# Performance work log

Measured on AMD Instinct MI355X. Metric: run time of the kernel, lower is better.

Reference implementation:

```python
import jax, jax.numpy as jnp
import numpy as np

N = 10000          # nodes
E_RAND = 320000    # random edges (avg degree 32)
F_IN = 512         # nfeat
HID = 256          # args.hid
HEADS = 8          # args.head
FH = HID // HEADS  # 32 per head
NCLASS = 40
TAU = 0.5
LAMDA = 0.5
K = 2


def setup_inputs() -> dict:
    key = jax.random.key(0)
    ks = jax.random.split(key, 16)
    # edge list: random edges + self-loops (so every dst segment is non-empty)
    src = jnp.concatenate([jax.random.randint(ks[0], (E_RAND,), 0, N), jnp.arange(N)])
    dst = jnp.concatenate([jax.random.randint(ks[1], (E_RAND,), 0, N), jnp.arange(N)])
    s = 0.05  # small init scale keeps exp() in attention/bind_loss stable
    return {
        "x": jax.random.normal(ks[2], (N, F_IN), jnp.float32),
        "src": src, "dst": dst,
        "W0": jax.random.normal(ks[3], (F_IN, HEADS, FH), jnp.float32) * s,
        "a0s": jax.random.normal(ks[4], (HEADS, FH), jnp.float32) * s,
        "a0d": jax.random.normal(ks[5], (HEADS, FH), jnp.float32) * s,
        "W1": jax.random.normal(ks[6], (HID, HEADS, FH), jnp.float32) * s,
        "a1s": jax.random.normal(ks[7], (HEADS, FH), jnp.float32) * s,
        "a1d": jax.random.normal(ks[8], (HEADS, FH), jnp.float32) * s,
        "W2": jax.random.normal(ks[9], (HID, HEADS, FH), jnp.float32) * s,
        "a2s": jax.random.normal(ks[10], (HEADS, FH), jnp.float32) * s,
        "a2d": jax.random.normal(ks[11], (HEADS, FH), jnp.float32) * s,
        "Wout": jax.random.normal(ks[12], (HID, HEADS, NCLASS), jnp.float32) * s,
        "aos": jax.random.normal(ks[13], (HEADS, NCLASS), jnp.float32) * s,
        "aod": jax.random.normal(ks[14], (HEADS, NCLASS), jnp.float32) * s,
    }


def _gat_layer(x, W, a_s, a_d, src, dst):
    """Sparse multi-head GAT layer: gather -> edge softmax -> scatter."""
    n = x.shape[0]
    h = jnp.einsum('nf,fhd->nhd', x, W)              # [N,H,Fh]
    es = jnp.sum(h * a_s, axis=-1)                    # [N,H]
    ed = jnp.sum(h * a_d, axis=-1)                    # [N,H]
    e = jax.nn.leaky_relu(es[src] + ed[dst], 0.2)     # [E,H]
    m = jax.ops.segment_max(e, dst, num_segments=n)   # per-dst max (stable softmax)
    w = jnp.exp(e - m[dst])
    z = jax.ops.segment_sum(w, dst, num_segments=n)
    alpha = w / z[dst]                                # [E,H]
    return jax.ops.segment_sum(alpha[:, :, None] * h[src], dst, num_segments=n)  # [N,H,Fh]


def _bind_loss(z):
    # z1 == z2 == z in the original call site: refl_sim == between_sim
    zn = z / jnp.maximum(jnp.linalg.norm(z, axis=1, keepdims=True), 1e-12)
    S = jnp.exp(jnp.matmul(zn, zn.T) / TAU)           # [N,N]
    d = jnp.diagonal(S)
    off = jnp.sum(S, axis=1) - d                      # masked (off-diagonal) row sum
    CT = -jnp.log(d / (off + off))                    # neg_c2.sum + neg_c3.sum
    return jnp.mean(CT)


def reference(x, src, dst, W0, a0s, a0d, W1, a1s, a1d, W2, a2s, a2d, Wout, aos, aod):
    layers = [(W0, a0s, a0d), (W1, a1s, a1d), (W2, a2s, a2d)]
    last = x
    loss = jnp.float32(0.0)
    for i, (W, as_, ad_) in enumerate(layers):
        cur = jax.nn.elu(_gat_layer(last, W, as_, ad_, src, dst))
        cur = cur.reshape(cur.shape[0], -1)           # concat heads -> [N, HID]
        if i > 0:
            beta = LAMDA / (i + 2)                    # MaskLayer(last, cur, lamda, i+2)
            cur = beta * last + (1.0 - beta) * cur
            if i % K == 0:
                loss = loss + _bind_loss(cur)
        last = cur
    out = _gat_layer(last, Wout, aos, aod, src, dst).mean(axis=1)  # avg heads -> [N,C]
    return (jax.nn.log_softmax(out, axis=1), loss)
```

## Files before the change

kernel.cpp:

```cpp
#include <hip/hip_runtime.h>
#include <hip/hip_bf16.h>
#include <math.h>

#define NN_F_IN   512
#define NN_HID    256
#define NN_HEADS  8
#define NN_FH     32
#define NN_NCLASS 40
#define TAU_F     0.5f
#define LAMDA_F   0.5f
#define ZN_SCALE  1.6986436f

typedef __attribute__((ext_vector_type(8))) short bf16x8;
typedef __attribute__((ext_vector_type(4))) float f32x4;

typedef __attribute__((address_space(1))) unsigned int gu32_t;
typedef __attribute__((address_space(3))) unsigned int lu32_t;

static __device__ __forceinline__ float lrelu02(float x) { return x >= 0.f ? x : 0.2f * x; }
static __device__ __forceinline__ float elu1(float x)    { return x > 0.f ? x : expm1f(x); }
static __device__ __forceinline__ float b2f(unsigned short u) {
    unsigned int x = ((unsigned int)u) << 16;
    return __uint_as_float(x);
}
static __device__ __forceinline__ unsigned short f2b(float f) {
    __hip_bfloat16 hb = __float2bfloat16(f);
    return *reinterpret_cast<unsigned short*>(&hb);
}

__global__ void prep_kernel(const float* __restrict__ x,
                            const float* __restrict__ W0, const float* __restrict__ W1,
                            const float* __restrict__ W2, const float* __restrict__ Wo,
                            unsigned short* __restrict__ Xb,
                            unsigned short* __restrict__ Wt0, unsigned short* __restrict__ Wt1,
                            unsigned short* __restrict__ Wt2, unsigned short* __restrict__ Wto,
                            int n4X) {
    int i = blockIdx.x * 256 + threadIdx.x;
    if (i < n4X) {
        float4 v = *(const float4*)(x + (size_t)i * 4);
        ushort4 o;
        o.x = f2b(v.x); o.y = f2b(v.y); o.z = f2b(v.z); o.w = f2b(v.w);
        *(ushort4*)(Xb + (size_t)i * 4) = o;
        return;
    }
    i -= n4X;
    if (i < 256 * 512) {
        int np = i >> 9, k = i & 511;
        Wt0[i] = f2b(W0[(size_t)k * 256 + np]);
        return;
    }
    i -= 256 * 512;
    if (i < 256 * 256) {
        int np = i >> 8, k = i & 255;
        Wt1[i] = f2b(W1[(size_t)k * 256 + np]);
        return;
    }
    i -= 256 * 256;
    if (i < 256 * 256) {
        int np = i >> 8, k = i & 255;
        Wt2[i] = f2b(W2[(size_t)k * 256 + np]);
        return;
    }
    i -= 256 * 256;
    if (i < 384 * 256) {
        int np = i >> 8, k = i & 255;
        Wto[i] = f2b(np < 320 ? Wo[(size_t)k * 320 + np] : 0.f);
    }
}

__global__ __launch_bounds__(256) void fc_attn_mfma(
    const unsigned short* __restrict__ A, const unsigned short* __restrict__ B,
    unsigned short* __restrict__ H, const float* __restrict__ As_,
    const float* __restrict__ Ad_, float* __restrict__ es, float* __restrict__ ed,
    int M, int K) {
    const int ldH = 256;
    int t = threadIdx.x, lane = t & 63, wid = t >> 6;
    int wrow = wid >> 1, wcol = wid & 1;
    int l15 = lane & 15, lg = lane >> 4;
    int mbase = blockIdx.y * 64 + wrow * 32;
    int nbase = blockIdx.x * 64 + wcol * 32;

    const unsigned short* Ap[2];
    const unsigned short* Bp[2];
#pragma unroll
    for (int m = 0; m < 2; ++m) {
        int rr = mbase + m * 16 + l15;
        if (rr > M - 1) rr = M - 1;
        Ap[m] = A + (size_t)rr * K + lg * 8;
        Bp[m] = B + (size_t)(nbase + m * 16 + l15) * K + lg * 8;
    }
    f32x4 acc[2][2];
#pragma unroll
    for (int m = 0; m < 2; ++m)
#pragma unroll
        for (int nn = 0; nn < 2; ++nn)
#pragma unroll
            for (int r = 0; r < 4; ++r) acc[m][nn][r] = 0.f;

    bf16x8 aP[2], bP[2], aQ[2], bQ[2];
#pragma unroll
    for (int m = 0; m < 2; ++m) {
        aP[m] = *(const bf16x8*)(Ap[m]);
        bP[m] = *(const bf16x8*)(Bp[m]);
    }
    int nhalf = K >> 6;
    int kk = 32;
    for (int it = 0; it < nhalf; ++it) {
#pragma unroll
        for (int m = 0; m < 2; ++m) {
            aQ[m] = *(const bf16x8*)(Ap[m] + kk);
            bQ[m] = *(const bf16x8*)(Bp[m] + kk);
        }
#pragma unroll
        for (int m = 0; m < 2; ++m)
#pragma unroll
            for (int nn = 0; nn < 2; ++nn)
                acc[m][nn] = __builtin_amdgcn_mfma_f32_16x16x32_bf16(aP[m], bP[nn], acc[m][nn], 0, 0, 0);
        if (it + 1 < nhalf) {
#pragma unroll
            for (int m = 0; m < 2; ++m) {
                aP[m] = *(const bf16x8*)(Ap[m] + kk + 32);
                bP[m] = *(const bf16x8*)(Bp[m] + kk + 32);
            }
        }
#pragma unroll
        for (int m = 0; m < 2; ++m)
#pragma unroll
            for (int nn = 0; nn < 2; ++nn)
                acc[m][nn] = __builtin_amdgcn_mfma_f32_16x16x32_bf16(aQ[m], bQ[nn], acc[m][nn], 0, 0, 0);
        kk += 64;
    }
#pragma unroll
    for (int m = 0; m < 2; ++m) {
#pragma unroll
        for (int nn = 0; nn < 2; ++nn) {
            int col = nbase + nn * 16 + l15;
#pragma unroll
            for (int r = 0; r < 4; ++r) {
                int row = mbase + m * 16 + lg * 4 + r;
                if (row < M) H[(size_t)row * ldH + col] = f2b(acc[m][nn][r]);
            }
        }
    }
    int hh = blockIdx.x * 2 + wcol;
    float a0 = As_[hh * 32 + l15], a1 = As_[hh * 32 + 16 + l15];
    float d0 = Ad_[hh * 32 + l15], d1 = Ad_[hh * 32 + 16 + l15];
#pragma unroll
    for (int m = 0; m < 2; ++m) {
#pragma unroll
        for (int r = 0; r < 4; ++r) {
            float ps = acc[m][0][r] * a0 + acc[m][1][r] * a1;
            float pd = acc[m][0][r] * d0 + acc[m][1][r] * d1;
            ps += __shfl_xor(ps, 1, 64); pd += __shfl_xor(pd, 1, 64);
            ps += __shfl_xor(ps, 2, 64); pd += __shfl_xor(pd, 2, 64);
            ps += __shfl_xor(ps, 4, 64); pd += __shfl_xor(pd, 4, 64);
            ps += __shfl_xor(ps, 8, 64); pd += __shfl_xor(pd, 8, 64);
            if (l15 == 0) {
                int row = mbase + m * 16 + lg * 4 + r;
                if (row < M) {
                    es[row * NN_HEADS + hh] = ps;
                    ed[row * NN_HEADS + hh] = pd;
                }
            }
        }
    }
}

__global__ __launch_bounds__(256) void fc_mfma(const unsigned short* __restrict__ A,
                                               const unsigned short* __restrict__ B,
                                               unsigned short* __restrict__ H,
                                               int M, int K, int ncols, int ldH) {
    int t = threadIdx.x, lane = t & 63, wid = t >> 6;
    int wrow = wid >> 1, wcol = wid & 1;
    int l15 = lane & 15, lg = lane >> 4;
    int mbase = blockIdx.y * 64 + wrow * 32;
    int nbase = blockIdx.x * 64 + wcol * 32;

    const unsigned short* Ap[2];
    const unsigned short* Bp[2];
#pragma unroll
    for (int m = 0; m < 2; ++m) {
        int rr = mbase + m * 16 + l15;
        if (rr > M - 1) rr = M - 1;
        Ap[m] = A + (size_t)rr * K + lg * 8;
        Bp[m] = B + (size_t)(nbase + m * 16 + l15) * K + lg * 8;
    }
    f32x4 acc[2][2];
#pragma unroll
    for (int m = 0; m < 2; ++m)
#pragma unroll
        for (int nn = 0; nn < 2; ++nn)
#pragma unroll
            for (int r = 0; r < 4; ++r) acc[m][nn][r] = 0.f;

    bf16x8 aP[2], bP[2], aQ[2], bQ[2];
#pragma unroll
    for (int m = 0; m < 2; ++m) {
        aP[m] = *(const bf16x8*)(Ap[m]);
        bP[m] = *(const bf16x8*)(Bp[m]);
    }
    int nhalf = K >> 6;
    int kk = 32;
    for (int it = 0; it < nhalf; ++it) {
#pragma unroll
        for (int m = 0; m < 2; ++m) {
            aQ[m] = *(const bf16x8*)(Ap[m] + kk);
            bQ[m] = *(const bf16x8*)(Bp[m] + kk);
        }
#pragma unroll
        for (int m = 0; m < 2; ++m)
#pragma unroll
            for (int nn = 0; nn < 2; ++nn)
                acc[m][nn] = __builtin_amdgcn_mfma_f32_16x16x32_bf16(aP[m], bP[nn], acc[m][nn], 0, 0, 0);
        if (it + 1 < nhalf) {
#pragma unroll
            for (int m = 0; m < 2; ++m) {
                aP[m] = *(const bf16x8*)(Ap[m] + kk + 32);
                bP[m] = *(const bf16x8*)(Bp[m] + kk + 32);
            }
        }
#pragma unroll
        for (int m = 0; m < 2; ++m)
#pragma unroll
            for (int nn = 0; nn < 2; ++nn)
                acc[m][nn] = __builtin_amdgcn_mfma_f32_16x16x32_bf16(aQ[m], bQ[nn], acc[m][nn], 0, 0, 0);
        kk += 64;
    }
#pragma unroll
    for (int m = 0; m < 2; ++m) {
#pragma unroll
        for (int nn = 0; nn < 2; ++nn) {
            int col = nbase + nn * 16 + l15;
            if (col >= ncols) continue;
#pragma unroll
            for (int r = 0; r < 4; ++r) {
                int row = mbase + m * 16 + lg * 4 + r;
                if (row < M) H[(size_t)row * ldH + col] = f2b(acc[m][nn][r]);
            }
        }
    }
}

__global__ void attn_kernel(const unsigned short* __restrict__ Hm, const float* __restrict__ As,
                            const float* __restrict__ Ad, float* __restrict__ es,
                            float* __restrict__ ed, int n, int df) {
    int idx = blockIdx.x * blockDim.x + threadIdx.x;
    if (idx >= n * NN_HEADS) return;
    int nn = idx / NN_HEADS, hh = idx - nn * NN_HEADS;
    const unsigned short* hp = Hm + (size_t)nn * NN_HEADS * df + hh * df;
    const float* ap = As + hh * df;
    const float* bp = Ad + hh * df;
    float s1 = 0.f, s2 = 0.f;
    for (int d = 0; d < df; d += 4) {
        ushort4 hv = *(const ushort4*)(hp + d);
        float4 av = *(const float4*)(ap + d);
        float4 bv = *(const float4*)(bp + d);
        float h0 = b2f(hv.x), h1 = b2f(hv.y), h2 = b2f(hv.z), h3 = b2f(hv.w);
        s1 += h0 * av.x + h1 * av.y + h2 * av.z + h3 * av.w;
        s2 += h0 * bv.x + h1 * bv.y + h2 * bv.z + h3 * bv.w;
    }
    es[idx] = s1;
    ed[idx] = s2;
}

__global__ __launch_bounds__(256) void edge_wz(
    const float* __restrict__ es, const float* __restrict__ ed,
    const int* __restrict__ csr_src, const int* __restrict__ row_start,
    float* __restrict__ wC, float* __restrict__ zinv, int n) {
    int lane = threadIdx.x & 63;
    int nn   = blockIdx.x * 4 + (threadIdx.x >> 6);
    if (nn >= n) return;
    int s0 = row_start[nn], s1 = row_start[nn + 1];
    int h    = lane & 7;
    int slot = lane >> 3;
    float edh = ed[nn * NN_HEADS + h];
    float z = 0.f;
    for (int e = s0 + slot; e < s1; e += 8) {
        int sv = csr_src[e];
        float w = __expf(lrelu02(es[sv * NN_HEADS + h] + edh));
        wC[(size_t)e * NN_HEADS + h] = w;
        z += w;
    }
    z += __shfl_xor(z, 8, 64);
    z += __shfl_xor(z, 16, 64);
    z += __shfl_xor(z, 32, 64);
    if (slot == 0) zinv[nn * NN_HEADS + h] = 1.f / z;
}

__global__ void count_kernel(const int* __restrict__ dst, int* __restrict__ counts, int E) {
    int e = blockIdx.x * blockDim.x + threadIdx.x;
    if (e < E) atomicAdd(&counts[dst[e]], 1);
}

__global__ void scan_kernel(const int* __restrict__ counts, int* __restrict__ row_start,
                            int* __restrict__ cursor, int n) {
    __shared__ int s[1024];
    int t  = threadIdx.x;
    int ch = (n + 1023) / 1024;
    int lo = t * ch;
    int sum = 0;
    for (int j = 0; j < ch; ++j) {
        int i = lo + j;
        if (i < n) sum += counts[i];
    }
    s[t] = sum;
    __syncthreads();
    for (int off = 1; off < 1024; off <<= 1) {
        int v = 0;
        if (t >= off) v = s[t - off];
        __syncthreads();
        s[t] += v;
        __syncthreads();
    }
    int run = (t == 0) ? 0 : s[t - 1];
    for (int j = 0; j < ch; ++j) {
        int i = lo + j;
        if (i < n) {
            row_start[i] = run;
            cursor[i] = run;
            run += counts[i];
        }
    }
    if (t == 1023) row_start[n] = s[1023];
}

__global__ void scatter_kernel(const int* __restrict__ src, const int* __restrict__ dst,
                               int* __restrict__ cursor, int* __restrict__ csr_src, int E) {
    int e = blockIdx.x * blockDim.x + threadIdx.x;
    if (e < E) {
        int d   = dst[e];
        int pos = atomicAdd(&cursor[d], 1);
        csr_src[pos] = src[e];
    }
}

__global__ __launch_bounds__(256) void gather_hidden(
    const unsigned short* __restrict__ Hm, const float* __restrict__ es,
    const float* __restrict__ ed, const int* __restrict__ csr_src,
    const int* __restrict__ row_start, const unsigned short* __restrict__ last,
    unsigned short* __restrict__ out, int n, float beta,
    unsigned short* __restrict__ znb, float* __restrict__ dvec) {
    int lane = threadIdx.x & 63;
    int nn   = blockIdx.x * 4 + (threadIdx.x >> 6);
    if (nn >= n) return;
    int s0 = row_start[nn], s1 = row_start[nn + 1];
    int h2 = lane >> 3;
    float edh = ed[nn * NN_HEADS + h2];

    float zacc = 0.f;
    float a0 = 0.f, a1 = 0.f, a2 = 0.f, a3 = 0.f;
    int fullEnd = s0 + ((s1 - s0) & ~7);
    int e = s0;
    for (; e < fullEnd; e += 8) {
        int idx[8];
        float q[8];
#pragma unroll
        for (int j = 0; j < 8; ++j) idx[j] = csr_src[e + j];
#pragma unroll
        for (int j = 0; j < 8; ++j) q[j] = es[idx[j] * NN_HEADS + h2];
        ushort4 r[8];
#pragma unroll
        for (int j = 0; j < 8; ++j) r[j] = *(const ushort4*)&Hm[(size_t)idx[j] * NN_HID + lane * 4];
#pragma unroll
        for (int j = 0; j < 8; ++j) {
            float w = __expf(lrelu02(q[j] + edh));
            zacc += w;
            a0 += w * b2f(r[j].x); a1 += w * b2f(r[j].y);
            a2 += w * b2f(r[j].z); a3 += w * b2f(r[j].w);
        }
    }
    if (e < s1) {
        int c = s1 - e;
        int idx[8];
        float q[8];
#pragma unroll
        for (int j = 0; j < 8; ++j) idx[j] = csr_src[(j < c) ? e + j : e];
#pragma unroll
        for (int j = 0; j < 8; ++j) q[j] = es[idx[j] * NN_HEADS + h2];
        ushort4 r[8];
#pragma unroll
        for (int j = 0; j < 8; ++j) r[j] = *(const ushort4*)&Hm[(size_t)idx[j] * NN_HID + lane * 4];
#pragma unroll
        for (int j = 0; j < 8; ++j) {
            if (j < c) {
                float w = __expf(lrelu02(q[j] + edh));
                zacc += w;
                a0 += w * b2f(r[j].x); a1 += w * b2f(r[j].y);
                a2 += w * b2f(r[j].z); a3 += w * b2f(r[j].w);
            }
        }
    }
    float zi = 1.f / zacc;
    float v0 = elu1(a0 * zi), v1 = elu1(a1 * zi), v2 = elu1(a2 * zi), v3 = elu1(a3 * zi);
    if (beta >= 0.f) {
        ushort4 lv = *(const ushort4*)&last[(size_t)nn * NN_HID + lane * 4];
        v0 = beta * b2f(lv.x) + (1.f - beta) * v0;
        v1 = beta * b2f(lv.y) + (1.f - beta) * v1;
        v2 = beta * b2f(lv.z) + (1.f - beta) * v2;
        v3 = beta * b2f(lv.w) + (1.f - beta) * v3;
    }
    ushort4 o;
    o.x = f2b(v0); o.y = f2b(v1); o.z = f2b(v2); o.w = f2b(v3);
    *(ushort4*)&out[(size_t)nn * NN_HID + lane * 4] = o;

    if (znb) {
        float ss = v0 * v0 + v1 * v1 + v2 * v2 + v3 * v3;
        ss += __shfl_xor(ss, 1, 64);
        ss += __shfl_xor(ss, 2, 64);
        ss += __shfl_xor(ss, 4, 64);
        ss += __shfl_xor(ss, 8, 64);
        ss += __shfl_xor(ss, 16, 64);
        ss += __shfl_xor(ss, 32, 64);
        float m = fmaxf(sqrtf(ss), 1e-12f);
        float sc = ZN_SCALE / m;
        ushort4 zo;
        zo.x = f2b(v0 * sc); zo.y = f2b(v1 * sc);
        zo.z = f2b(v2 * sc); zo.w = f2b(v3 * sc);
        *(ushort4*)&znb[(size_t)nn * NN_HID + lane * 4] = zo;
        if (lane == 0) dvec[nn] = __expf((ss / (m * m)) * (1.f / TAU_F));
    }
}

__global__ void gather_final(const unsigned short* __restrict__ Hm, const float* __restrict__ wC,
                             const float* __restrict__ zinv, const int* __restrict__ csr_src,
                             const int* __restrict__ row_start, float* __restrict__ dout, int n) {
    int nn = blockIdx.x;
    __shared__ float accs[NN_HEADS * NN_NCLASS];
    int t = threadIdx.x;
    int s0 = row_start[nn], s1 = row_start[nn + 1];
    int hh = t / NN_NCLASS;
    float acc = 0.f;
    const int LD = NN_HEADS * NN_NCLASS;
    int fullEnd = s0 + ((s1 - s0) & ~7);
    int e = s0;
    for (; e < fullEnd; e += 8) {
        int idx[8];
        float wv[8];
#pragma unroll
        for (int j = 0; j < 8; ++j) {
            idx[j] = csr_src[e + j];
            wv[j]  = wC[(size_t)(e + j) * NN_HEADS + hh];
        }
        float v[8];
#pragma unroll
        for (int j = 0; j < 8; ++j) v[j] = b2f(Hm[(size_t)idx[j] * LD + t]);
#pragma unroll
        for (int j = 0; j < 8; ++j) acc += wv[j] * v[j];
    }
    if (e < s1) {
        int c = s1 - e;
        int idx[8];
        float wv[8];
#pragma unroll
        for (int j = 0; j < 8; ++j) {
            int p = (j < c) ? e + j : e;
            idx[j] = csr_src[p];
            wv[j]  = wC[(size_t)p * NN_HEADS + hh];
        }
        float v[8];
#pragma unroll
        for (int j = 0; j < 8; ++j) v[j] = b2f(Hm[(size_t)idx[j] * LD + t]);
#pragma unroll
        for (int j = 0; j < 8; ++j) {
            if (j < c) acc += wv[j] * v[j];
        }
    }
    accs[t] = acc * zinv[nn * NN_HEADS + hh];
    __syncthreads();
    if (t < 64) {
        float v = -INFINITY;
        if (t < NN_NCLASS) {
            float sacc = 0.f;
#pragma unroll
            for (int h2 = 0; h2 < NN_HEADS; ++h2) sacc += accs[h2 * NN_NCLASS + t];
            v = sacc * (1.f / NN_HEADS);
        }
        float mx = v;
#pragma unroll
        for (int o = 1; o < 64; o <<= 1) mx = fmaxf(mx, __shfl_xor(mx, o, 64));
        float ex = (t < NN_NCLASS) ? expf(v - mx) : 0.f;
        float se = ex;
#pragma unroll
        for (int o = 1; o < 64; o <<= 1) se += __shfl_xor(se, o, 64);
        if (t < NN_NCLASS) dout[(size_t)nn * NN_NCLASS + t] = (v - mx) - logf(se);
    }
}

__global__ __launch_bounds__(256) void gram_mfma(const short* __restrict__ znb,
                                                 float* __restrict__ P2d, int n,
                                                 int T, int nwg, int Npad) {
    __shared__ short As[2][128 * 32];
    __shared__ short Bs[2][128 * 32];

    int b = blockIdx.x;
    int q = nwg >> 3, r8 = nwg & 7, xc = b & 7, oo = b >> 3;
    int sid = (xc < r8 ? xc * (q + 1) : r8 * (q + 1) + (xc - r8) * q) + oo;
    int bi = 0, rem = sid;
    while (rem >= T - bi) { rem -= T - bi; ++bi; }
    int bj = bi + rem;
    int i0 = bi * 128, j0 = bj * 128;

    int t    = threadIdx.x;
    int lane = t & 63;
    int wid  = t >> 6;
    int wrow = wid >> 1, wcol = wid & 1;
    int l15  = lane & 15, lg = lane >> 4;

    int srow0 = 16 * (2 * wid + 0) + (lane >> 2);
    int srow1 = 16 * (2 * wid + 1) + (lane >> 2);
    int kc    = lane & 3;
    int kc0   = kc ^ ((srow0 >> 1) & 3);
    int kc1   = kc ^ ((srow1 >> 1) & 3);
    const short* gA0 = znb + (size_t)(i0 + srow0) * NN_HID + kc0 * 8;
    const short* gA1 = znb + (size_t)(i0 + srow1) * NN_HID + kc1 * 8;
    const short* gB0 = znb + (size_t)(j0 + srow0) * NN_HID + kc0 * 8;
    const short* gB1 = znb + (size_t)(j0 + srow1) * NN_HID + kc1 * 8;
    int ldst0 = (2 * wid + 0) * 512 + lane * 8;
    int ldst1 = (2 * wid + 1) * 512 + lane * 8;

    auto stage = [&](int buf, int s) {
        int ko = s * 32;
        __builtin_amdgcn_global_load_lds((gu32_t*)(gA0 + ko), (lu32_t*)(&As[buf][ldst0]), 16, 0, 0);
        __builtin_amdgcn_global_load_lds((gu32_t*)(gA1 + ko), (lu32_t*)(&As[buf][ldst1]), 16, 0, 0);
        __builtin_amdgcn_global_load_lds((gu32_t*)(gB0 + ko), (lu32_t*)(&Bs[buf][ldst0]), 16, 0, 0);
        __builtin_amdgcn_global_load_lds((gu32_t*)(gB1 + ko), (lu32_t*)(&Bs[buf][ldst1]), 16, 0, 0);
    };

    f32x4 acc[4][4];
#pragma unroll
    for (int m = 0; m < 4; ++m)
#pragma unroll
        for (int nn = 0; nn < 4; ++nn)
#pragma unroll
            for (int r = 0; r < 4; ++r) acc[m][nn][r] = 0.f;

    stage(0, 0);
    __syncthreads();
#pragma unroll
    for (int s = 0; s < 8; ++s) {
        int cur = s & 1;
        if (s < 7) stage(cur ^ 1, s + 1);
        bf16x8 av[4], bv[4];
#pragma unroll
        for (int m = 0; m < 4; ++m) {
            int Ra = wrow * 64 + m * 16 + l15;
            int ca = lg ^ ((Ra >> 1) & 3);
            av[m] = *(const bf16x8*)&As[cur][Ra * 32 + ca * 8];
        }
#pragma unroll
        for (int m = 0; m < 4; ++m) {
            int Rb = wcol * 64 + m * 16 + l15;
            int cb = lg ^ ((Rb >> 1) & 3);
            bv[m] = *(const bf16x8*)&Bs[cur][Rb * 32 + cb * 8];
        }
#pragma unroll
        for (int m = 0; m < 4; ++m)
#pragma unroll
            for (int nn = 0; nn < 4; ++nn)
                acc[m][nn] = __builtin_amdgcn_mfma_f32_16x16x32_bf16(av[m], bv[nn], acc[m][nn], 0, 0, 0);
        __syncthreads();
    }

    int i0w = i0 + wrow * 64;
    int j0w = j0 + wcol * 64;
    bool diag = (bj == bi);
    if (bj == T - 1) {
#pragma unroll
        for (int m = 0; m < 4; ++m)
#pragma unroll
            for (int nn = 0; nn < 4; ++nn) {
                int gj = j0w + nn * 16 + l15;
                bool jok = gj < n;
#pragma unroll
                for (int r = 0; r < 4; ++r) {
                    int gi = i0w + m * 16 + lg * 4 + r;
                    acc[m][nn][r] = (jok && gi < n) ? __builtin_exp2f(acc[m][nn][r]) : 0.f;
                }
            }
    } else {
#pragma unroll
        for (int m = 0; m < 4; ++m)
#pragma unroll
            for (int nn = 0; nn < 4; ++nn)
#pragma unroll
                for (int r = 0; r < 4; ++r)
                    acc[m][nn][r] = __builtin_exp2f(acc[m][nn][r]);
    }
    float* rowslot = P2d + (size_t)(2 * bj + wcol) * Npad;
#pragma unroll
    for (int m = 0; m < 4; ++m) {
#pragma unroll
        for (int r = 0; r < 4; ++r) {
            float v = acc[m][0][r] + acc[m][1][r] + acc[m][2][r] + acc[m][3][r];
            v += __shfl_xor(v, 1, 64);
            v += __shfl_xor(v, 2, 64);
            v += __shfl_xor(v, 4, 64);
            v += __shfl_xor(v, 8, 64);
            if (l15 == 0) {
                int gi = i0w + m * 16 + lg * 4 + r;
                if (gi < n) rowslot[gi] = v;
            }
        }
    }
    if (!diag) {
        float* colslot = P2d + (size_t)(2 * bi + wrow) * Npad;
#pragma unroll
        for (int nn = 0; nn < 4; ++nn) {
            float v = 0.f;
#pragma unroll
            for (int m = 0; m < 4; ++m)
#pragma unroll
                for (int r = 0; r < 4; ++r) v += acc[m][nn][r];
            v += __shfl_xor(v, 16, 64);
            v += __shfl_xor(v, 32, 64);
            if (lg == 0) {
                int gj = j0w + nn * 16 + l15;
                if (gj < n) colslot[gj] = v;
            }
        }
    }
}

__global__ void fold_kernel(const float* __restrict__ P2d, float* __restrict__ R,
                            int n, int slots, int Npad) {
    int i = blockIdx.x * 256 + threadIdx.x;
    if (i >= n) return;
    const float* p = P2d + i;
    float s0 = 0.f, s1 = 0.f, s2 = 0.f, s3 = 0.f;
    int sl = 0;
    for (; sl + 4 <= slots; sl += 4) {
        s0 += p[(size_t)(sl + 0) * Npad];
        s1 += p[(size_t)(sl + 1) * Npad];
        s2 += p[(size_t)(sl + 2) * Npad];
        s3 += p[(size_t)(sl + 3) * Npad];
    }
    for (; sl < slots; ++sl) s0 += p[(size_t)sl * Npad];
    R[i] = (s0 + s1) + (s2 + s3);
}

__global__ void loss_kernel(const float* __restrict__ R, const float* __restrict__ dvec,
                            float* __restrict__ out_loss, int n) {
    __shared__ float s[1024];
    int t = threadIdx.x;
    float sum = 0.f;
    for (int i = t; i < n; i += 1024) {
        float d   = dvec[i];
        float off = R[i] - d;
        sum += -logf(d / (off + off));
    }
    s[t] = sum;
    __syncthreads();
    for (int o = 512; o > 0; o >>= 1) {
        if (t < o) s[t] += s[t + o];
        __syncthreads();
    }
    if (t == 0) *out_loss = s[0] / n;
}

extern "C" void kernel_launch(void* const* d_in, const int* in_sizes, int n_in,
                              void* d_out, int out_size, void* d_ws, size_t ws_size,
                              hipStream_t stream) {
    const float* x   = (const float*)d_in[0];
    const int*   src = (const int*)d_in[1];
    const int*   dst = (const int*)d_in[2];
    const float* W0  = (const float*)d_in[3];
    const float* a0s = (const float*)d_in[4];
    const float* a0d = (const float*)d_in[5];
    const float* W1  = (const float*)d_in[6];
    const float* a1s = (const float*)d_in[7];
    const float* a1d = (const float*)d_in[8];
    const float* W2  = (const float*)d_in[9];
    const float* a2s = (const float*)d_in[10];
    const float* a2d = (const float*)d_in[11];
    const float* Wout= (const float*)d_in[12];
    const float* aos = (const float*)d_in[13];
    const float* aod = (const float*)d_in[14];

    int N = in_sizes[0] / NN_F_IN;
    int E = in_sizes[1];
    int Npad = ((N + 127) / 128) * 128;
    int T = Npad / 128;
    int nwg = T * (T + 1) / 2;
    float* out = (float*)d_out;

    char*  ws  = (char*)d_ws;
    size_t off = 0;
    auto alloc = [&](size_t bytes) -> void* {
        void* p = ws + off;
        off += bytes;
        off = (off + 255) & ~(size_t)255;
        return p;
    };
    unsigned short* Hb = (unsigned short*)alloc((size_t)N * 320 * 2);
    unsigned short* znb = (unsigned short*)alloc((size_t)Npad * NN_HID * 2);
    unsigned short* Bl = (unsigned short*)alloc((size_t)N * NN_HID * 2);
    unsigned short* Bc = (unsigned short*)alloc((size_t)N * NN_HID * 2);
    size_t xbBytes = (size_t)N * NN_F_IN * 2;
    size_t p2Bytes = (size_t)2 * T * Npad * 4;
    void* XbP2d = alloc(xbBytes > p2Bytes ? xbBytes : p2Bytes);
    unsigned short* Xb  = (unsigned short*)XbP2d;
    float*          P2d = (float*)XbP2d;
    unsigned short* Wt0 = (unsigned short*)alloc((size_t)256 * 512 * 2);
    unsigned short* Wt1 = (unsigned short*)alloc((size_t)256 * 256 * 2);
    unsigned short* Wt2 = (unsigned short*)alloc((size_t)256 * 256 * 2);
    unsigned short* Wto = (unsigned short*)alloc((size_t)384 * 256 * 2);
    float* es     = (float*)alloc((size_t)N * NN_HEADS * 4);
    float* ed     = (float*)alloc((size_t)N * NN_HEADS * 4);
    float* wC     = (float*)alloc((size_t)E * NN_HEADS * 4);
    float* zinvA  = (float*)alloc((size_t)N * NN_HEADS * 4);
    float* Rrow   = (float*)alloc((size_t)N * 4);
    float* dvec   = (float*)alloc((size_t)N * 4);
    int*   counts = (int*)alloc((size_t)N * 4);
    int*   rs     = (int*)alloc((size_t)(N + 1) * 4);
    int*   cursor = (int*)alloc((size_t)N * 4);
    int*   csr    = (int*)alloc((size_t)E * 4);

    hipMemsetAsync(counts, 0, (size_t)N * 4, stream);
    if (Npad > N)
        hipMemsetAsync(znb + (size_t)N * NN_HID, 0, (size_t)(Npad - N) * NN_HID * 2, stream);
    count_kernel<<<(E + 255) / 256, 256, 0, stream>>>(dst, counts, E);
    scan_kernel<<<1, 1024, 0, stream>>>(counts, rs, cursor, N);
    scatter_kernel<<<(E + 255) / 256, 256, 0, stream>>>(src, dst, cursor, csr, E);

    int n4X = N * NN_F_IN / 4;
    int prepTotal = n4X + 256 * 512 + 256 * 256 + 256 * 256 + 384 * 256;
    prep_kernel<<<(prepTotal + 255) / 256, 256, 0, stream>>>(
        x, W0, W1, W2, Wout, Xb, Wt0, Wt1, Wt2, Wto, n4X);

    int atGrid = (N * NN_HEADS + 255) / 256;
    int ghGrid = (N + 3) / 4;
    int mT64 = (N + 63) / 64;

    fc_attn_mfma<<<dim3(4, mT64), 256, 0, stream>>>(Xb, Wt0, Hb, a0s, a0d, es, ed, N, 512);
    gather_hidden<<<ghGrid, 256, 0, stream>>>(Hb, es, ed, csr, rs, nullptr, Bl, N, -1.f,
                                              nullptr, nullptr);

    fc_attn_mfma<<<dim3(4, mT64), 256, 0, stream>>>(Bl, Wt1, Hb, a1s, a1d, es, ed, N, 256);
    gather_hidden<<<ghGrid, 256, 0, stream>>>(Hb, es, ed, csr, rs, Bl, Bc, N, LAMDA_F / 3.f,
                                              nullptr, nullptr);

    fc_attn_mfma<<<dim3(4, mT64), 256, 0, stream>>>(Bc, Wt2, Hb, a2s, a2d, es, ed, N, 256);
    gather_hidden<<<ghGrid, 256, 0, stream>>>(Hb, es, ed, csr, rs, Bc, Bl, N, LAMDA_F / 4.f,
                                              znb, dvec);

    gram_mfma<<<nwg, 256, 0, stream>>>((const short*)znb, P2d, N, T, nwg, Npad);
    fold_kernel<<<(N + 255) / 256, 256, 0, stream>>>(P2d, Rrow, N, 2 * T, Npad);
    loss_kernel<<<1, 1024, 0, stream>>>(Rrow, dvec, out + (size_t)N * NN_NCLASS, N);

    fc_mfma<<<dim3(5, mT64), 256, 0, stream>>>(Bl, Wto, Hb, N, 256, 320, 320);
    attn_kernel<<<atGrid, 256, 0, stream>>>(Hb, aos, aod, es, ed, N, NN_NCLASS);
    edge_wz<<<ghGrid, 256, 0, stream>>>(es, ed, csr, rs, wC, zinvA, N);
    gather_final<<<N, NN_HEADS * NN_NCLASS, 0, stream>>>(Hb, wC, zinvA, csr, rs, out, N);
}
```

Before: 366.9 us.

## Widen gather unroll to 16 edges and restage gram tiles through registers

The gather_hidden and gather_final loops now process 16 edges per iteration instead of 8, giving more independent loads in flight per thread. The gram MFMA kernel drops its direct global-to-LDS async copies over 8 k-steps of 32. It now loads 64-wide k slabs into registers, writes them to swizzled LDS, and prefetches the second half while computing the first, which halves the number of barriers. The cost is higher register pressure, a larger LDS footprint per block (64 KB) that may lower occupancy, and more wasted work in the tail for low-degree rows.

```diff
diff --git a/kernel.cpp b/kernel.cpp
--- a/kernel.cpp
+++ b/kernel.cpp
@@ -13,9 +13,6 @@
 
 typedef __attribute__((ext_vector_type(8))) short bf16x8;
 typedef __attribute__((ext_vector_type(4))) float f32x4;
-
-typedef __attribute__((address_space(1))) unsigned int gu32_t;
-typedef __attribute__((address_space(3))) unsigned int lu32_t;
 
 static __device__ __forceinline__ float lrelu02(float x) { return x >= 0.f ? x : 0.2f * x; }
 static __device__ __forceinline__ float elu1(float x)    { return x > 0.f ? x : expm1f(x); }
@@ -349,20 +346,20 @@
 
     float zacc = 0.f;
     float a0 = 0.f, a1 = 0.f, a2 = 0.f, a3 = 0.f;
-    int fullEnd = s0 + ((s1 - s0) & ~7);
+    int fullEnd = s0 + ((s1 - s0) & ~15);
     int e = s0;
-    for (; e < fullEnd; e += 8) {
-        int idx[8];
-        float q[8];
-#pragma unroll
-        for (int j = 0; j < 8; ++j) idx[j] = csr_src[e + j];
-#pragma unroll
-        for (int j = 0; j < 8; ++j) q[j] = es[idx[j] * NN_HEADS + h2];
-        ushort4 r[8];
-#pragma unroll
-        for (int j = 0; j < 8; ++j) r[j] = *(const ushort4*)&Hm[(size_t)idx[j] * NN_HID + lane * 4];
-#pragma unroll
-        for (int j = 0; j < 8; ++j) {
+    for (; e < fullEnd; e += 16) {
+        int idx[16];
+        float q[16];
+#pragma unroll
+        for (int j = 0; j < 16; ++j) idx[j] = csr_src[e + j];
+#pragma unroll
+        for (int j = 0; j < 16; ++j) q[j] = es[idx[j] * NN_HEADS + h2];
+        ushort4 r[16];
+#pragma unroll
+        for (int j = 0; j < 16; ++j) r[j] = *(const ushort4*)&Hm[(size_t)idx[j] * NN_HID + lane * 4];
+#pragma unroll
+        for (int j = 0; j < 16; ++j) {
             float w = __expf(lrelu02(q[j] + edh));
             zacc += w;
             a0 += w * b2f(r[j].x); a1 += w * b2f(r[j].y);
@@ -371,17 +368,17 @@
     }
     if (e < s1) {
         int c = s1 - e;
-        int idx[8];
-        float q[8];
-#pragma unroll
-        for (int j = 0; j < 8; ++j) idx[j] = csr_src[(j < c) ? e + j : e];
-#pragma unroll
-        for (int j = 0; j < 8; ++j) q[j] = es[idx[j] * NN_HEADS + h2];
-        ushort4 r[8];
-#pragma unroll
-        for (int j = 0; j < 8; ++j) r[j] = *(const ushort4*)&Hm[(size_t)idx[j] * NN_HID + lane * 4];
-#pragma unroll
-        for (int j = 0; j < 8; ++j) {
+        int idx[16];
+        float q[16];
+#pragma unroll
+        for (int j = 0; j < 16; ++j) idx[j] = csr_src[(j < c) ? e + j : e];
+#pragma unroll
+        for (int j = 0; j < 16; ++j) q[j] = es[idx[j] * NN_HEADS + h2];
+        ushort4 r[16];
+#pragma unroll
+        for (int j = 0; j < 16; ++j) r[j] = *(const ushort4*)&Hm[(size_t)idx[j] * NN_HID + lane * 4];
+#pragma unroll
+        for (int j = 0; j < 16; ++j) {
             if (j < c) {
                 float w = __expf(lrelu02(q[j] + edh));
                 zacc += w;
@@ -431,37 +428,37 @@
     int hh = t / NN_NCLASS;
     float acc = 0.f;
     const int LD = NN_HEADS * NN_NCLASS;
-    int fullEnd = s0 + ((s1 - s0) & ~7);
+    int fullEnd = s0 + ((s1 - s0) & ~15);
     int e = s0;
-    for (; e < fullEnd; e += 8) {
-        int idx[8];
-        float wv[8];
-#pragma unroll
-        for (int j = 0; j < 8; ++j) {
+    for (; e < fullEnd; e += 16) {
+        int idx[16];
+        float wv[16];
+#pragma unroll
+        for (int j = 0; j < 16; ++j) {
             idx[j] = csr_src[e + j];
             wv[j]  = wC[(size_t)(e + j) * NN_HEADS + hh];
         }
-        float v[8];
-#pragma unroll
-        for (int j = 0; j < 8; ++j) v[j] = b2f(Hm[(size_t)idx[j] * LD + t]);
-#pragma unroll
-        for (int j = 0; j < 8; ++j) acc += wv[j] * v[j];
+        float v[16];
+#pragma unroll
+        for (int j = 0; j < 16; ++j) v[j] = b2f(Hm[(size_t)idx[j] * LD + t]);
+#pragma unroll
+        for (int j = 0; j < 16; ++j) acc += wv[j] * v[j];
     }
     if (e < s1) {
         int c = s1 - e;
-        int idx[8];
-        float wv[8];
-#pragma unroll
-        for (int j = 0; j < 8; ++j) {
+        int idx[16];
+        float wv[16];
+#pragma unroll
+        for (int j = 0; j < 16; ++j) {
             int p = (j < c) ? e + j : e;
             idx[j] = csr_src[p];
             wv[j]  = wC[(size_t)p * NN_HEADS + hh];
         }
-        float v[8];
-#pragma unroll
-        for (int j = 0; j < 8; ++j) v[j] = b2f(Hm[(size_t)idx[j] * LD + t]);
-#pragma unroll
-        for (int j = 0; j < 8; ++j) {
+        float v[16];
+#pragma unroll
+        for (int j = 0; j < 16; ++j) v[j] = b2f(Hm[(size_t)idx[j] * LD + t]);
+#pragma unroll
+        for (int j = 0; j < 16; ++j) {
             if (j < c) acc += wv[j] * v[j];
         }
     }
@@ -489,8 +486,8 @@
 __global__ __launch_bounds__(256) void gram_mfma(const short* __restrict__ znb,
                                                  float* __restrict__ P2d, int n,
                                                  int T, int nwg, int Npad) {
-    __shared__ short As[2][128 * 32];
-    __shared__ short Bs[2][128 * 32];
+    __shared__ short As[2][128 * 64];
+    __shared__ short Bs[2][128 * 64];
 
     int b = blockIdx.x;
     int q = nwg >> 3, r8 = nwg & 7, xc = b & 7, oo = b >> 3;
@@ -505,26 +502,8 @@
     int wid  = t >> 6;
     int wrow = wid >> 1, wcol = wid & 1;
     int l15  = lane & 15, lg = lane >> 4;
-
-    int srow0 = 16 * (2 * wid + 0) + (lane >> 2);
-    int srow1 = 16 * (2 * wid + 1) + (lane >> 2);
-    int kc    = lane & 3;
-    int kc0   = kc ^ ((srow0 >> 1) & 3);
-    int kc1   = kc ^ ((srow1 >> 1) & 3);
-    const short* gA0 = znb + (size_t)(i0 + srow0) * NN_HID + kc0 * 8;
-    const short* gA1 = znb + (size_t)(i0 + srow1) * NN_HID + kc1 * 8;
-    const short* gB0 = znb + (size_t)(j0 + srow0) * NN_HID + kc0 * 8;
-    const short* gB1 = znb + (size_t)(j0 + srow1) * NN_HID + kc1 * 8;
-    int ldst0 = (2 * wid + 0) * 512 + lane * 8;
-    int ldst1 = (2 * wid + 1) * 512 + lane * 8;
-
-    auto stage = [&](int buf, int s) {
-        int ko = s * 32;
-        __builtin_amdgcn_global_load_lds((gu32_t*)(gA0 + ko), (lu32_t*)(&As[buf][ldst0]), 16, 0, 0);
-        __builtin_amdgcn_global_load_lds((gu32_t*)(gA1 + ko), (lu32_t*)(&As[buf][ldst1]), 16, 0, 0);
-        __builtin_amdgcn_global_load_lds((gu32_t*)(gB0 + ko), (lu32_t*)(&Bs[buf][ldst0]), 16, 0, 0);
-        __builtin_amdgcn_global_load_lds((gu32_t*)(gB1 + ko), (lu32_t*)(&Bs[buf][ldst1]), 16, 0, 0);
-    };
+    int srow = lane >> 3;
+    int sch  = lane & 7;
 
     f32x4 acc[4][4];
 #pragma unroll
@@ -534,31 +513,61 @@
 #pragma unroll
             for (int r = 0; r < 4; ++r) acc[m][nn][r] = 0.f;
 
-    stage(0, 0);
-    __syncthreads();
-#pragma unroll
-    for (int s = 0; s < 8; ++s) {
-        int cur = s & 1;
-        if (s < 7) stage(cur ^ 1, s + 1);
-        bf16x8 av[4], bv[4];
-#pragma unroll
-        for (int m = 0; m < 4; ++m) {
-            int Ra = wrow * 64 + m * 16 + l15;
-            int ca = lg ^ ((Ra >> 1) & 3);
-            av[m] = *(const bf16x8*)&As[cur][Ra * 32 + ca * 8];
-        }
-#pragma unroll
-        for (int m = 0; m < 4; ++m) {
-            int Rb = wcol * 64 + m * 16 + l15;
-            int cb = lg ^ ((Rb >> 1) & 3);
-            bv[m] = *(const bf16x8*)&Bs[cur][Rb * 32 + cb * 8];
-        }
-#pragma unroll
-        for (int m = 0; m < 4; ++m)
-#pragma unroll
-            for (int nn = 0; nn < 4; ++nn)
-                acc[m][nn] = __builtin_amdgcn_mfma_f32_16x16x32_bf16(av[m], bv[nn], acc[m][nn], 0, 0, 0);
+    bf16x8 sa[2][4], sb[2][4];
+#pragma unroll
+    for (int sl = 0; sl < 2; ++sl)
+#pragma unroll
+        for (int s = 0; s < 4; ++s) {
+            int row = wid * 32 + s * 8 + srow;
+            int gch = sch ^ (row & 7);
+            sa[sl][s] = *(const bf16x8*)(znb + (size_t)(i0 + row) * NN_HID + sl * 64 + gch * 8);
+            sb[sl][s] = *(const bf16x8*)(znb + (size_t)(j0 + row) * NN_HID + sl * 64 + gch * 8);
+        }
+
+#pragma unroll
+    for (int kt = 0; kt < 2; ++kt) {
+#pragma unroll
+        for (int sl = 0; sl < 2; ++sl)
+#pragma unroll
+            for (int s = 0; s < 4; ++s) {
+                int row = wid * 32 + s * 8 + srow;
+                *(bf16x8*)(&As[sl][row * 64 + sch * 8]) = sa[sl][s];
+                *(bf16x8*)(&Bs[sl][row * 64 + sch * 8]) = sb[sl][s];
+            }
         __syncthreads();
+        if (kt == 0) {
+#pragma unroll
+            for (int sl = 0; sl < 2; ++sl)
+#pragma unroll
+                for (int s = 0; s < 4; ++s) {
+                    int row = wid * 32 + s * 8 + srow;
+                    int gch = sch ^ (row & 7);
+                    sa[sl][s] = *(const bf16x8*)(znb + (size_t)(i0 + row) * NN_HID + 128 + sl * 64 + gch * 8);
+                    sb[sl][s] = *(const bf16x8*)(znb + (size_t)(j0 + row) * NN_HID + 128 + sl * 64 + gch * 8);
+                }
+        }
+#pragma unroll
+        for (int sl = 0; sl < 2; ++sl) {
+#pragma unroll
+            for (int ks = 0; ks < 2; ++ks) {
+                bf16x8 av[4], bv[4];
+#pragma unroll
+                for (int m = 0; m < 4; ++m) {
+                    int Ra = wrow * 64 + m * 16 + l15;
+                    int Rb = wcol * 64 + m * 16 + l15;
+                    int ca = (ks * 4 + lg) ^ (Ra & 7);
+                    int cb = (ks * 4 + lg) ^ (Rb & 7);
+                    av[m] = *(const bf16x8*)(&As[sl][Ra * 64 + ca * 8]);
+                    bv[m] = *(const bf16x8*)(&Bs[sl][Rb * 64 + cb * 8]);
+                }
+#pragma unroll
+                for (int m = 0; m < 4; ++m)
+#pragma unroll
+                    for (int nn = 0; nn < 4; ++nn)
+                        acc[m][nn] = __builtin_amdgcn_mfma_f32_16x16x32_bf16(av[m], bv[nn], acc[m][nn], 0, 0, 0);
+            }
+        }
+        if (kt == 0) __syncthreads();
     }
 
     int i0w = i0 + wrow * 64;
```

After: 375.5 us. +2.4%, slower.
